# Kernel tuning notes

Measured on AMD Instinct MI355X. Metric: run time of the kernel, lower is better.

Reference implementation:

```python
import jax, jax.numpy as jnp
import numpy as np

D = 64          # embedding_dim
B = 1024        # batch (queries)
R = 128         # num_relations
N = 100000      # num_nodes
E = 6400000     # num_edges


def setup_inputs() -> dict:
    key = jax.random.key(0)
    ks = jax.random.split(key, 16)
    inp = {
        "relation_embeddings": jax.random.normal(ks[0], (B, R, D), dtype=jnp.float32),
        "query_rels": jax.random.randint(ks[1], (B,), 0, R),
        "query_entities": jax.random.randint(ks[2], (B,), 0, N),
        "edge_index": jax.random.randint(ks[3], (2, E), 0, N),
        "edge_type": jax.random.randint(ks[4], (E,), 0, R),
        "num_nodes": N,
        # feature_extractor: Linear(2D+4 -> D), ReLU, Linear(D -> D//2), ReLU
        "W1": jax.random.normal(ks[5], (2 * D + 4, D), dtype=jnp.float32) * 0.05,
        "b1": jnp.zeros((D,), dtype=jnp.float32),
        "W2": jax.random.normal(ks[6], (D, D // 2), dtype=jnp.float32) * 0.05,
        "b2": jnp.zeros((D // 2,), dtype=jnp.float32),
        # gate_network: Linear(D//2 -> D//4), ReLU, Linear(D//4 -> 1), Sigmoid
        "Wg1": jax.random.normal(ks[7], (D // 2, D // 4), dtype=jnp.float32) * 0.05,
        "bg1": jnp.zeros((D // 4,), dtype=jnp.float32),
        "Wg2": jax.random.normal(ks[8], (D // 4, 1), dtype=jnp.float32) * 0.05,
        "bg2": jnp.full((1,), 0.85, dtype=jnp.float32),
    }
    return inp


def reference(relation_embeddings, query_rels, query_entities, edge_index,
              edge_type, num_nodes, W1, b1, W2, b2, Wg1, bg1, Wg2, bg2):
    b, r, d = relation_embeddings.shape
    e = edge_type.shape[0]
    e_f = jnp.float32(e)
    src, dst = edge_index[0], edge_index[1]
    # count self-loop edges once (matches boolean OR mask in torch code)
    not_loop = (src != dst).astype(jnp.float32)

    # --- graph statistics (vectorized replacement of per-query masks) ---
    rel_counts = jnp.zeros((r,), jnp.float32).at[edge_type].add(1.0)          # [R]
    rel_freq_norm = jnp.minimum(rel_counts[query_rels] / e_f, 1.0)            # [B]

    deg = (jnp.zeros((num_nodes,), jnp.float32)
           .at[src].add(1.0).at[dst].add(not_loop))                           # [N]
    deg_q = deg[query_entities]                                               # [B]
    entity_degree_norm = jnp.minimum(deg_q / e_f, 1.0)

    density = jnp.minimum(e_f / jnp.float32(num_nodes * num_nodes), 1.0)
    stats = jnp.stack([rel_freq_norm, entity_degree_norm, rel_freq_norm,
                       jnp.full_like(rel_freq_norm, density)], axis=-1)       # [B,4]

    # --- query relation embedding ---
    rel_emb = relation_embeddings[jnp.arange(b), query_rels]                  # [B,D]

    # --- entity embedding = mean of relation embeddings over incident edges ---
    # per-node histogram of incident edge types (self loops counted once)
    hist = (jnp.zeros((num_nodes, r), jnp.float32)
            .at[src, edge_type].add(1.0)
            .at[dst, edge_type].add(not_loop))                                # [N,R]
    Mq = hist[query_entities]                                                 # [B,R]
    ent_sum = jnp.einsum('br,brd->bd', Mq, relation_embeddings)               # [B,D]
    entity_emb = ent_sum / jnp.maximum(deg_q, 1.0)[:, None]                   # zeros if deg==0

    # --- gated MLP ---
    feat = jnp.concatenate([rel_emb, entity_emb, stats], axis=-1)             # [B,2D+4]
    h = jax.nn.relu(feat @ W1 + b1)
    h = jax.nn.relu(h @ W2 + b2)
    g = jax.nn.relu(h @ Wg1 + bg1)
    gate = jax.nn.sigmoid(g @ Wg2 + bg2)[:, 0]                                # [B]
    return gate
```

## Files before the change

### kernel.cpp

```cpp
#include <hip/hip_runtime.h>
#include <math.h>


#define NNODES 100000
#define NWORDS ((NNODES + 31) / 32)
#define NWP    (((NWORDS + 3) / 4) * 4)
#define RR     128
#define DD     64
#define FF     (2 * DD + 4)
#define E4C    1600000
#define EDGE_BLOCKS 1536
#define EDGE_THREADS 256
#define NTC    (EDGE_BLOCKS * EDGE_THREADS)
#define HITCAP 768
#define SETUP_BLOCKS 256

__global__ void zero_kernel(int4* __restrict__ p, int n4)
{
    int i = blockIdx.x * blockDim.x + threadIdx.x;
    int stride = gridDim.x * blockDim.x;
    int4 z = make_int4(0, 0, 0, 0);
    for (int k = i; k < n4; k += stride) p[k] = z;
}

__global__ void __launch_bounds__(1024)
setup_kernel(const int* __restrict__ qents, int B,
             unsigned* __restrict__ gmask, int* __restrict__ gbase,
             const int* __restrict__ etype, int E,
             int* __restrict__ relcnt)
{
    int t = threadIdx.x;
    if (blockIdx.x != 0) {
        __shared__ int s_cnt[RR];
        if (t < RR) s_cnt[t] = 0;
        __syncthreads();
        int ne4 = E >> 2;
        const int4* et4 = (const int4*)etype;
        int i = (blockIdx.x - 1) * 1024 + t;
        int stride = (SETUP_BLOCKS - 1) * 1024;
        for (int k = i; k < ne4; k += stride) {
            int4 ty = et4[k];
            atomicAdd(&s_cnt[ty.x], 1);
            atomicAdd(&s_cnt[ty.y], 1);
            atomicAdd(&s_cnt[ty.z], 1);
            atomicAdd(&s_cnt[ty.w], 1);
        }
        if (blockIdx.x == 1) {
            for (int e = (ne4 << 2) + t; e < E; e += 1024)
                atomicAdd(&s_cnt[etype[e]], 1);
        }
        __syncthreads();
        if (t < RR) {
            int c = s_cnt[t];
            if (c) atomicAdd(&relcnt[t], c);
        }
        return;
    }
    __shared__ unsigned s_mask[NWP];
    __shared__ int s_wsum[16], s_wbase[16];
    for (int k = t; k < NWP; k += 1024) s_mask[k] = 0u;
    __syncthreads();
    for (int b = t; b < B; b += 1024) {
        int e = qents[b];
        atomicOr(&s_mask[e >> 5], 1u << (e & 31));
    }
    __syncthreads();
    int w0 = t * 4;
    int pc[4]; int sum = 0;
#pragma unroll
    for (int k = 0; k < 4; ++k) {
        int w = w0 + k;
        unsigned mm = (w < NWP) ? s_mask[w] : 0u;
        pc[k] = __popc(mm);
        sum += pc[k];
    }
    int lane = t & 63, wid = t >> 6;
    int incl = sum;
#pragma unroll
    for (int off = 1; off < 64; off <<= 1) {
        int v = __shfl_up(incl, off);
        if (lane >= off) incl += v;
    }
    if (lane == 63) s_wsum[wid] = incl;
    __syncthreads();
    if (t == 0) {
        int run = 0;
#pragma unroll
        for (int k = 0; k < 16; ++k) { s_wbase[k] = run; run += s_wsum[k]; }
    }
    __syncthreads();
    int base = s_wbase[wid] + incl - sum;
#pragma unroll
    for (int k = 0; k < 4; ++k) {
        int w = w0 + k;
        if (w < NWP) gbase[w] = base;
        base += pc[k];
    }
    for (int k = t; k < NWP; k += 1024) gmask[k] = s_mask[k];
}

static __device__ __forceinline__ void hitrec(
    int node, int e,
    const unsigned* s_mask, const int* __restrict__ gbase,
    unsigned* s_hnode, unsigned* s_hedge, int* s_hn,
    int* __restrict__ Mslot, const int* __restrict__ etype)
{
    unsigned w = s_mask[node >> 5];
    if ((w >> (node & 31)) & 1u) {
        int idx = atomicAdd(s_hn, 1);
        if (idx < HITCAP) {
            s_hnode[idx] = (unsigned)node;
            s_hedge[idx] = (unsigned)e;
        } else {
            int slot = gbase[node >> 5] + __popc(w & ((1u << (node & 31)) - 1u));
            atomicAdd(&Mslot[slot * RR + etype[e]], 1);
        }
    }
}

static __device__ __forceinline__ void edge4s(
    int4 s, int4 d, int i,
    const unsigned* s_mask, const int* __restrict__ gbase,
    unsigned* s_hnode, unsigned* s_hedge, int* s_hn,
    int* __restrict__ Mslot, const int* __restrict__ etype)
{
    int e = i * 4;
    hitrec(s.x, e + 0, s_mask, gbase, s_hnode, s_hedge, s_hn, Mslot, etype);
    if (s.x != d.x) hitrec(d.x, e + 0, s_mask, gbase, s_hnode, s_hedge, s_hn, Mslot, etype);
    hitrec(s.y, e + 1, s_mask, gbase, s_hnode, s_hedge, s_hn, Mslot, etype);
    if (s.y != d.y) hitrec(d.y, e + 1, s_mask, gbase, s_hnode, s_hedge, s_hn, Mslot, etype);
    hitrec(s.z, e + 2, s_mask, gbase, s_hnode, s_hedge, s_hn, Mslot, etype);
    if (s.z != d.z) hitrec(d.z, e + 2, s_mask, gbase, s_hnode, s_hedge, s_hn, Mslot, etype);
    hitrec(s.w, e + 3, s_mask, gbase, s_hnode, s_hedge, s_hn, Mslot, etype);
    if (s.w != d.w) hitrec(d.w, e + 3, s_mask, gbase, s_hnode, s_hedge, s_hn, Mslot, etype);
}

__global__ void __launch_bounds__(EDGE_THREADS, 6)
edge_kernel(const int* __restrict__ ei, const int* __restrict__ etype,
            int E, int E4,
            const unsigned* __restrict__ gmask, const int* __restrict__ gbase,
            int* __restrict__ Mslot)
{
    __shared__ __align__(16) unsigned s_mask[NWP];
    __shared__ unsigned s_hnode[HITCAP];
    __shared__ unsigned s_hedge[HITCAP];
    __shared__ int s_hn;
    int t = threadIdx.x;
    if (t == 0) s_hn = 0;
    const uint4* gm4 = (const uint4*)gmask;
    for (int i = t; i < NWP / 4; i += EDGE_THREADS)
        ((uint4*)s_mask)[i] = gm4[i];
    __syncthreads();

    int tid  = blockIdx.x * EDGE_THREADS + t;
    int nthr = gridDim.x * EDGE_THREADS;

    const int4* src4 = (const int4*)ei;
    const int4* dst4 = (const int4*)(ei + E);

    if (E4 == E4C && nthr == NTC) {
        int i0 = tid, i1 = tid + NTC, i2 = tid + 2 * NTC, i3 = tid + 3 * NTC;
        int4 s0 = src4[i0], d0 = dst4[i0];
        int4 s1 = src4[i1], d1 = dst4[i1];
        int4 s2 = src4[i2], d2 = dst4[i2];
        int4 s3 = src4[i3], d3 = dst4[i3];
        __builtin_amdgcn_sched_barrier(0);
        edge4s(s0, d0, i0, s_mask, gbase, s_hnode, s_hedge, &s_hn, Mslot, etype);
        edge4s(s1, d1, i1, s_mask, gbase, s_hnode, s_hedge, &s_hn, Mslot, etype);
        edge4s(s2, d2, i2, s_mask, gbase, s_hnode, s_hedge, &s_hn, Mslot, etype);
        edge4s(s3, d3, i3, s_mask, gbase, s_hnode, s_hedge, &s_hn, Mslot, etype);
        int i4 = tid + 4 * NTC;
        if (i4 < E4C) {
            int4 s4 = src4[i4], d4 = dst4[i4];
            edge4s(s4, d4, i4, s_mask, gbase, s_hnode, s_hedge, &s_hn, Mslot, etype);
        }
    } else {
        for (int i = tid; i < E4; i += nthr) {
            int4 s = src4[i], d = dst4[i];
            edge4s(s, d, i, s_mask, gbase, s_hnode, s_hedge, &s_hn, Mslot, etype);
        }
        for (int e = (E4 << 2) + tid; e < E; e += nthr) {
            int s = ei[e], d = ei[E + e];
            hitrec(s, e, s_mask, gbase, s_hnode, s_hedge, &s_hn, Mslot, etype);
            if (s != d)
                hitrec(d, e, s_mask, gbase, s_hnode, s_hedge, &s_hn, Mslot, etype);
        }
    }

    __syncthreads();
    int hn = s_hn; if (hn > HITCAP) hn = HITCAP;
    for (int i = t; i < hn; i += EDGE_THREADS) {
        int node = (int)s_hnode[i];
        int e    = (int)s_hedge[i];
        unsigned w = s_mask[node >> 5];
        int slot = gbase[node >> 5] + __popc(w & ((1u << (node & 31)) - 1u));
        atomicAdd(&Mslot[slot * RR + etype[e]], 1);
    }
}

__global__ void query_kernel(
    const float* __restrict__ RE,
    const int* __restrict__ qrels, const int* __restrict__ qents,
    const int* __restrict__ relcnt, const int* __restrict__ Mslot,
    const unsigned* __restrict__ gmask, const int* __restrict__ gbase,
    const float* __restrict__ W1, const float* __restrict__ b1,
    const float* __restrict__ W2, const float* __restrict__ b2,
    const float* __restrict__ Wg1, const float* __restrict__ bg1,
    const float* __restrict__ Wg2, const float* __restrict__ bg2,
    float* __restrict__ out, float e_f, float density)
{
    __shared__ float s_m[RR];
    __shared__ float s_part[256];
    __shared__ float s_feat[FF];
    __shared__ float s_h1[DD];
    __shared__ float s_h2[DD / 2];
    __shared__ float s_g[DD / 4];
    __shared__ int s_slot;

    int b = blockIdx.x;
    int t = threadIdx.x;
    int d = t & (DD - 1);
    int w = t >> 6;

    if (t == 0) {
        int e = qents[b];
        unsigned mm = gmask[e >> 5];
        s_slot = gbase[e >> 5] + __popc(mm & ((1u << (e & 31)) - 1u));
    }
    __syncthreads();
    int slot = s_slot;

    if (t < RR) s_m[t] = (float)Mslot[slot * RR + t];
    __syncthreads();

    const float* REb = RE + (size_t)b * RR * DD;
    float acc = 0.f;
#pragma unroll 8
    for (int r = w; r < RR; r += 4)
        acc = fmaf(s_m[r], REb[r * DD + d], acc);
    s_part[w * DD + d] = acc;
    __syncthreads();

    if (t < DD) {
        float ds = s_m[t] + s_m[t + DD];
#pragma unroll
        for (int off = 32; off > 0; off >>= 1) ds += __shfl_xor(ds, off);

        float ent = s_part[t] + s_part[DD + t] + s_part[2 * DD + t] + s_part[3 * DD + t];

        int qr = qrels[b];
        s_feat[t]      = REb[qr * DD + t];
        s_feat[DD + t] = ent / fmaxf(ds, 1.f);
        if (t == 0) {
            float rf = fminf((float)relcnt[qr] / e_f, 1.f);
            s_feat[2 * DD + 0] = rf;
            s_feat[2 * DD + 1] = fminf(ds / e_f, 1.f);
            s_feat[2 * DD + 2] = rf;
            s_feat[2 * DD + 3] = density;
        }
    }
    __syncthreads();

    {
        int c = t >> 6, n = t & 63;
        int i0 = c * 33;
        float a = 0.f;
#pragma unroll
        for (int k = 0; k < 33; ++k) {
            int i = i0 + k;
            a = fmaf(s_feat[i], W1[i * DD + n], a);
        }
        s_part[t] = a;
    }
    __syncthreads();
    if (t < DD) {
        float a = b1[t] + s_part[t] + s_part[64 + t] + s_part[128 + t] + s_part[192 + t];
        s_h1[t] = fmaxf(a, 0.f);
    }
    __syncthreads();

    {
        int c = t >> 5, n = t & 31;
        float a = 0.f;
#pragma unroll
        for (int k = 0; k < 8; ++k) {
            int i = c * 8 + k;
            a = fmaf(s_h1[i], W2[i * 32 + n], a);
        }
        s_part[t] = a;
    }
    __syncthreads();
    if (t < 32) {
        float a = b2[t];
#pragma unroll
        for (int c = 0; c < 8; ++c) a += s_part[c * 32 + t];
        s_h2[t] = fmaxf(a, 0.f);
    }
    __syncthreads();

    if (t < 16) {
        float a = bg1[t];
#pragma unroll
        for (int i = 0; i < 32; ++i) a = fmaf(s_h2[i], Wg1[i * 16 + t], a);
        s_g[t] = fmaxf(a, 0.f);
    }
    __syncthreads();

    if (t == 0) {
        float a = bg2[0];
#pragma unroll
        for (int i = 0; i < 16; ++i) a = fmaf(s_g[i], Wg2[i], a);
        out[b] = 1.f / (1.f + expf(-a));
    }
}

extern "C" void kernel_launch(void* const* d_in, const int* in_sizes, int n_in,
                              void* d_out, int out_size, void* d_ws, size_t ws_size,
                              hipStream_t stream)
{
    const float* RE    = (const float*)d_in[0];
    const int*   qrels = (const int*)d_in[1];
    const int*   qents = (const int*)d_in[2];
    const int*   ei    = (const int*)d_in[3];
    const int*   etype = (const int*)d_in[4];
    const float* W1  = (const float*)d_in[6];
    const float* b1  = (const float*)d_in[7];
    const float* W2  = (const float*)d_in[8];
    const float* b2  = (const float*)d_in[9];
    const float* Wg1 = (const float*)d_in[10];
    const float* bg1 = (const float*)d_in[11];
    const float* Wg2 = (const float*)d_in[12];
    const float* bg2 = (const float*)d_in[13];
    float* out = (float*)d_out;

    int B = in_sizes[1];
    int E = in_sizes[4];

    int* ws_i   = (int*)d_ws;
    int* Mslot  = ws_i;
    int* relcnt = Mslot + (size_t)B * RR;
    unsigned* mask = (unsigned*)(relcnt + RR);
    int* word_base = (int*)(mask + NWP);

    float e_f = (float)E;
    float density = fminf((float)E / ((float)NNODES * (float)NNODES), 1.f);

    int n4 = (B * RR + RR) / 4;
    zero_kernel<<<256, 256, 0, stream>>>((int4*)d_ws, n4);

    setup_kernel<<<SETUP_BLOCKS, 1024, 0, stream>>>(qents, B, mask, word_base,
                                                    etype, E, relcnt);

    int E4 = ((E & 3) == 0) ? (E >> 2) : 0;
    edge_kernel<<<EDGE_BLOCKS, EDGE_THREADS, 0, stream>>>(ei, etype, E, E4,
                                                          mask, word_base, Mslot);

    query_kernel<<<B, 256, 0, stream>>>(RE, qrels, qents, relcnt, Mslot,
                                        mask, word_base,
                                        W1, b1, W2, b2, Wg1, bg1, Wg2, bg2,
                                        out, e_f, density);
}
```

Before: 44.67 us.

## Merge zeroing into init kernel and fuse relation histogram into edge pass

Zeroing of the workspace is folded into the mask-setup kernel, and the edge-type histogram moves out of setup into extra blocks of the edge kernel, so both scans run concurrently in one launch and one launch is removed. The histogram now uses four sub-histograms per block to reduce shared-atomic contention. Hit capacity drops to 512, the load schedule is loosened, and the query kernel skips zero-weight relation rows. The risks are hit overflow with the smaller cap and occupancy changes in the combined kernel.

```diff
diff --git a/kernel.cpp b/kernel.cpp
--- a/kernel.cpp
+++ b/kernel.cpp
@@ -9,51 +9,23 @@
 #define DD     64
 #define FF     (2 * DD + 4)
 #define E4C    1600000
-#define EDGE_BLOCKS 1536
-#define EDGE_THREADS 256
-#define NTC    (EDGE_BLOCKS * EDGE_THREADS)
-#define HITCAP 768
-#define SETUP_BLOCKS 256
-
-__global__ void zero_kernel(int4* __restrict__ p, int n4)
-{
-    int i = blockIdx.x * blockDim.x + threadIdx.x;
-    int stride = gridDim.x * blockDim.x;
-    int4 z = make_int4(0, 0, 0, 0);
-    for (int k = i; k < n4; k += stride) p[k] = z;
-}
+#define HIST_BLOCKS 768
+#define EDGE_W      1536
+#define W_BLOCKS    (HIST_BLOCKS + EDGE_W)
+#define W_THREADS   256
+#define NTC    (EDGE_W * W_THREADS)
+#define HITCAP 512
+#define NHTHR  (HIST_BLOCKS * W_THREADS)
 
 __global__ void __launch_bounds__(1024)
-setup_kernel(const int* __restrict__ qents, int B,
-             unsigned* __restrict__ gmask, int* __restrict__ gbase,
-             const int* __restrict__ etype, int E,
-             int* __restrict__ relcnt)
+init_kernel(const int* __restrict__ qents, int B,
+            unsigned* __restrict__ gmask, int* __restrict__ gbase,
+            int4* __restrict__ zp, int n4)
 {
     int t = threadIdx.x;
     if (blockIdx.x != 0) {
-        __shared__ int s_cnt[RR];
-        if (t < RR) s_cnt[t] = 0;
-        __syncthreads();
-        int ne4 = E >> 2;
-        const int4* et4 = (const int4*)etype;
-        int i = (blockIdx.x - 1) * 1024 + t;
-        int stride = (SETUP_BLOCKS - 1) * 1024;
-        for (int k = i; k < ne4; k += stride) {
-            int4 ty = et4[k];
-            atomicAdd(&s_cnt[ty.x], 1);
-            atomicAdd(&s_cnt[ty.y], 1);
-            atomicAdd(&s_cnt[ty.z], 1);
-            atomicAdd(&s_cnt[ty.w], 1);
-        }
-        if (blockIdx.x == 1) {
-            for (int e = (ne4 << 2) + t; e < E; e += 1024)
-                atomicAdd(&s_cnt[etype[e]], 1);
-        }
-        __syncthreads();
-        if (t < RR) {
-            int c = s_cnt[t];
-            if (c) atomicAdd(&relcnt[t], c);
-        }
+        int zi = (blockIdx.x - 1) * 1024 + t;
+        if (zi < n4) zp[zi] = make_int4(0, 0, 0, 0);
         return;
     }
     __shared__ unsigned s_mask[NWP];
@@ -135,38 +107,67 @@
     if (s.w != d.w) hitrec(d.w, e + 3, s_mask, gbase, s_hnode, s_hedge, s_hn, Mslot, etype);
 }
 
-__global__ void __launch_bounds__(EDGE_THREADS, 6)
-edge_kernel(const int* __restrict__ ei, const int* __restrict__ etype,
+__global__ void __launch_bounds__(W_THREADS, 8)
+work_kernel(const int* __restrict__ ei, const int* __restrict__ etype,
             int E, int E4,
             const unsigned* __restrict__ gmask, const int* __restrict__ gbase,
-            int* __restrict__ Mslot)
+            int* __restrict__ Mslot, int* __restrict__ relcnt)
 {
     __shared__ __align__(16) unsigned s_mask[NWP];
     __shared__ unsigned s_hnode[HITCAP];
     __shared__ unsigned s_hedge[HITCAP];
+    __shared__ int s_cnt[4][RR];
     __shared__ int s_hn;
     int t = threadIdx.x;
+
+    if (blockIdx.x < HIST_BLOCKS) {
+        int sub = (t >> 6) & 3;
+        for (int i = t; i < 4 * RR; i += W_THREADS) ((int*)s_cnt)[i] = 0;
+        __syncthreads();
+        int hb = blockIdx.x;
+        int ne4 = E >> 2;
+        const int4* et4 = (const int4*)etype;
+        int i = hb * W_THREADS + t;
+        for (int k = i; k < ne4; k += NHTHR) {
+            int4 ty = et4[k];
+            atomicAdd(&s_cnt[sub][ty.x], 1);
+            atomicAdd(&s_cnt[sub][ty.y], 1);
+            atomicAdd(&s_cnt[sub][ty.z], 1);
+            atomicAdd(&s_cnt[sub][ty.w], 1);
+        }
+        if (hb == 0) {
+            for (int e = (ne4 << 2) + t; e < E; e += W_THREADS)
+                atomicAdd(&s_cnt[0][etype[e]], 1);
+        }
+        __syncthreads();
+        if (t < RR) {
+            int c = s_cnt[0][t] + s_cnt[1][t] + s_cnt[2][t] + s_cnt[3][t];
+            if (c) atomicAdd(&relcnt[t], c);
+        }
+        return;
+    }
+
     if (t == 0) s_hn = 0;
     const uint4* gm4 = (const uint4*)gmask;
-    for (int i = t; i < NWP / 4; i += EDGE_THREADS)
+    for (int i = t; i < NWP / 4; i += W_THREADS)
         ((uint4*)s_mask)[i] = gm4[i];
     __syncthreads();
 
-    int tid  = blockIdx.x * EDGE_THREADS + t;
-    int nthr = gridDim.x * EDGE_THREADS;
+    int eid  = blockIdx.x - HIST_BLOCKS;
+    int tid  = eid * W_THREADS + t;
+    int nthr = EDGE_W * W_THREADS;
 
     const int4* src4 = (const int4*)ei;
     const int4* dst4 = (const int4*)(ei + E);
 
-    if (E4 == E4C && nthr == NTC) {
+    if (E4 == E4C) {
         int i0 = tid, i1 = tid + NTC, i2 = tid + 2 * NTC, i3 = tid + 3 * NTC;
         int4 s0 = src4[i0], d0 = dst4[i0];
         int4 s1 = src4[i1], d1 = dst4[i1];
         int4 s2 = src4[i2], d2 = dst4[i2];
-        int4 s3 = src4[i3], d3 = dst4[i3];
-        __builtin_amdgcn_sched_barrier(0);
         edge4s(s0, d0, i0, s_mask, gbase, s_hnode, s_hedge, &s_hn, Mslot, etype);
         edge4s(s1, d1, i1, s_mask, gbase, s_hnode, s_hedge, &s_hn, Mslot, etype);
+        int4 s3 = src4[i3], d3 = dst4[i3];
         edge4s(s2, d2, i2, s_mask, gbase, s_hnode, s_hedge, &s_hn, Mslot, etype);
         edge4s(s3, d3, i3, s_mask, gbase, s_hnode, s_hedge, &s_hn, Mslot, etype);
         int i4 = tid + 4 * NTC;
@@ -189,7 +190,7 @@
 
     __syncthreads();
     int hn = s_hn; if (hn > HITCAP) hn = HITCAP;
-    for (int i = t; i < hn; i += EDGE_THREADS) {
+    for (int i = t; i < hn; i += W_THREADS) {
         int node = (int)s_hnode[i];
         int e    = (int)s_hedge[i];
         unsigned w = s_mask[node >> 5];
@@ -235,9 +236,11 @@
 
     const float* REb = RE + (size_t)b * RR * DD;
     float acc = 0.f;
-#pragma unroll 8
-    for (int r = w; r < RR; r += 4)
-        acc = fmaf(s_m[r], REb[r * DD + d], acc);
+#pragma unroll 4
+    for (int r = w; r < RR; r += 4) {
+        float m = s_m[r];
+        if (m != 0.f) acc = fmaf(m, REb[r * DD + d], acc);
+    }
     s_part[w * DD + d] = acc;
     __syncthreads();
 
@@ -346,14 +349,14 @@
     float density = fminf((float)E / ((float)NNODES * (float)NNODES), 1.f);
 
     int n4 = (B * RR + RR) / 4;
-    zero_kernel<<<256, 256, 0, stream>>>((int4*)d_ws, n4);
-
-    setup_kernel<<<SETUP_BLOCKS, 1024, 0, stream>>>(qents, B, mask, word_base,
-                                                    etype, E, relcnt);
+
+    init_kernel<<<65, 1024, 0, stream>>>(qents, B, mask, word_base,
+                                         (int4*)d_ws, n4);
 
     int E4 = ((E & 3) == 0) ? (E >> 2) : 0;
-    edge_kernel<<<EDGE_BLOCKS, EDGE_THREADS, 0, stream>>>(ei, etype, E, E4,
-                                                          mask, word_base, Mslot);
+    work_kernel<<<W_BLOCKS, W_THREADS, 0, stream>>>(ei, etype, E, E4,
+                                                    mask, word_base,
+                                                    Mslot, relcnt);
 
     query_kernel<<<B, 256, 0, stream>>>(RE, qrels, qents, relcnt, Mslot,
                                         mask, word_base,
```

New measurement: 56.13 us. 1.26x slower.
